# Kernel tuning notes

Measured on AMD Instinct MI355X. Metric: run time of the kernel, lower is better.

Reference implementation:

```python
import jax, jax.numpy as jnp
import numpy as np

N_NODES = 50000
N_EDGES = 800000
D_IN = 128
D_HID = 200
D_OUT = 64
EPS = 0.0  # initial_eps, train_eps=False


def setup_inputs() -> dict:
    key = jax.random.key(0)
    ks = jax.random.split(key, 8)
    x = jax.random.normal(ks[0], (N_NODES, D_IN), dtype=jnp.float32)
    edge_row = jax.random.randint(ks[1], (N_EDGES,), 0, N_NODES)
    edge_col = jax.random.randint(ks[2], (N_EDGES,), 0, N_NODES)
    edge_val = jax.random.uniform(ks[3], (N_EDGES,), dtype=jnp.float32)
    W1 = jax.random.normal(ks[4], (D_IN, D_HID), dtype=jnp.float32) * 0.05
    b1 = jnp.zeros((D_HID,), dtype=jnp.float32)
    W2 = jax.random.normal(ks[5], (D_HID, D_OUT), dtype=jnp.float32) * 0.05
    b2 = jnp.zeros((D_OUT,), dtype=jnp.float32)
    return {"x": x, "edge_row": edge_row, "edge_col": edge_col,
            "edge_val": edge_val, "W1": W1, "b1": b1, "W2": W2, "b2": b2}


def reference(x, edge_row, edge_col, edge_val, W1, b1, W2, b2):
    # SpMM: agg[i] = sum_e val[e] * x[col[e]] for edges with row[e] == i
    msgs = edge_val[:, None] * x[edge_col]            # [E, D_IN] gather
    agg = jax.ops.segment_sum(msgs, edge_row, num_segments=N_NODES)  # [N, D_IN]
    # (1 + eps) * x + A @ x, then 2-layer MLP (Linear -> ReLU -> Linear)
    h = (1.0 + EPS) * x + agg
    h = jax.nn.relu(h @ W1 + b1)                      # [N, D_HID]
    out = h @ W2 + b2                                 # [N, D_OUT]
    return out
```

## Files before the change

kernel.cpp:

```cpp
#include <hip/hip_runtime.h>

#define NN 50000
#define NE 800000
#define DIN 128
#define DH 200
#define DHP 256
#define DO 64
#define RPB 32
#define NBUCK 1564
#define CAP 1024
#define EPB 4096
#define NBLK_E ((NE + EPB - 1) / EPB)
#define CVT_B 3125
#define PACK_B 24

typedef float f32x4 __attribute__((ext_vector_type(4)));
typedef short bf16x8 __attribute__((ext_vector_type(8)));
typedef short s16x4 __attribute__((ext_vector_type(4)));
typedef unsigned int uint;

__device__ __forceinline__ unsigned short f2bf(float f) {
  unsigned int b = __float_as_uint(f);
  b = (b + 0x7FFFu + ((b >> 16) & 1u)) >> 16;
  return (unsigned short)b;
}
__device__ __forceinline__ float bf2f(unsigned short u) {
  return __uint_as_float((unsigned int)u << 16);
}

__global__ __launch_bounds__(256) void k_prep(const float* __restrict__ x,
                                              uint* __restrict__ xb,
                                              const int* __restrict__ row,
                                              int* __restrict__ hist,
                                              const float* __restrict__ W1,
                                              const float* __restrict__ W2,
                                              unsigned short* __restrict__ B1p,
                                              unsigned short* __restrict__ B2p) {
  __shared__ int lh[NBUCK];
  const int bid = blockIdx.x;
  const int tid = threadIdx.x;
  if (bid < CVT_B) {
    int i = bid * 256 + tid;
    f32x4 a = *reinterpret_cast<const f32x4*>(x + (size_t)i * 8);
    f32x4 b = *reinterpret_cast<const f32x4*>(x + (size_t)i * 8 + 4);
    uint4 o;
    o.x = (uint)f2bf(a[0]) | ((uint)f2bf(a[1]) << 16);
    o.y = (uint)f2bf(a[2]) | ((uint)f2bf(a[3]) << 16);
    o.z = (uint)f2bf(b[0]) | ((uint)f2bf(b[1]) << 16);
    o.w = (uint)f2bf(b[2]) | ((uint)f2bf(b[3]) << 16);
    *reinterpret_cast<uint4*>(xb + (size_t)i * 4) = o;
  } else if (bid < CVT_B + NBLK_E) {
    const int hb = bid - CVT_B;
    const int e0 = hb * EPB;
    for (int j = tid; j < NBUCK; j += 256) lh[j] = 0;
    __syncthreads();
#pragma unroll
    for (int p = 0; p < EPB / 256; ++p) {
      int e = e0 + p * 256 + tid;
      if (e < NE) atomicAdd(&lh[row[e] / RPB], 1);
    }
    __syncthreads();
    int* hrow = hist + (size_t)hb * NBUCK;
    for (int j = tid; j < NBUCK; j += 256) hrow[j] = lh[j];
  } else {
    int gidx = (bid - CVT_B - NBLK_E) * 256 + tid;
    if (gidx < 4096) {
      int idx = gidx;
      int lane = idx & 63;
      int s = (idx >> 6) & 3;
      int t = idx >> 8;
      int n = t * 16 + (lane & 15);
      unsigned short v[8];
#pragma unroll
      for (int j = 0; j < 8; ++j) {
        int k = s * 32 + (j & 3) + ((lane >> 4) << 2) + ((j >> 2) << 4);
        float f = (n < DH) ? W1[(size_t)k * DH + n] : 0.f;
        v[j] = f2bf(f);
      }
      *reinterpret_cast<uint4*>(B1p + (size_t)idx * 8) =
          *reinterpret_cast<const uint4*>(v);
    } else {
      int idx = gidx - 4096;
      int lane = idx & 63;
      int s = (idx >> 6) & 7;
      int t = idx >> 9;
      int n = t * 16 + (lane & 15);
      unsigned short v[8];
#pragma unroll
      for (int j = 0; j < 8; ++j) {
        int k = s * 32 + (j & 3) + ((lane >> 4) << 2) + ((j >> 2) << 4);
        float f = (k < DH) ? W2[(size_t)k * DO + n] : 0.f;
        v[j] = f2bf(f);
      }
      *reinterpret_cast<uint4*>(B2p + (size_t)idx * 8) =
          *reinterpret_cast<const uint4*>(v);
    }
  }
}

__global__ __launch_bounds__(256) void k_scanB(int* __restrict__ hist,
                                               int* __restrict__ cnt) {
  __shared__ int ws[4];
  const int k = blockIdx.x;
  const int tid = threadIdx.x;
  int v = (tid < NBLK_E) ? hist[(size_t)tid * NBUCK + k] : 0;
  int lane = tid & 63, wid = tid >> 6;
  int incl = v;
#pragma unroll
  for (int d = 1; d < 64; d <<= 1) {
    int t = __shfl_up(incl, d, 64);
    if (lane >= d) incl += t;
  }
  if (lane == 63) ws[wid] = incl;
  __syncthreads();
  if (tid == 0) {
    int s = 0;
#pragma unroll
    for (int q = 0; q < 4; ++q) { int xx = ws[q]; ws[q] = s; s += xx; }
  }
  __syncthreads();
  int excl = ws[wid] + incl - v;
  if (tid < NBLK_E) hist[(size_t)tid * NBUCK + k] = excl;
  if (tid == 255) cnt[k] = excl;
}

__global__ __launch_bounds__(256) void k_scatC(const int* __restrict__ row,
                                               const int* __restrict__ col,
                                               const float* __restrict__ val,
                                               const int* __restrict__ hist,
                                               uint2* __restrict__ ep) {
  __shared__ int lh[NBUCK];
  __shared__ int lbase[NBUCK];
  const int tid = threadIdx.x;
  const int e0 = blockIdx.x * EPB;
  const int* hrow = hist + (size_t)blockIdx.x * NBUCK;
  for (int j = tid; j < NBUCK; j += 256) { lh[j] = 0; lbase[j] = hrow[j]; }
  __syncthreads();
#pragma unroll
  for (int p = 0; p < EPB / 256; ++p) {
    int e = e0 + p * 256 + tid;
    if (e < NE) {
      int r = row[e];
      int k = r / RPB;
      int rank = atomicAdd(&lh[k], 1);
      int pos = lbase[k] + rank;
      if (pos < CAP)
        ep[(size_t)k * CAP + pos] =
            make_uint2((uint)col[e] | ((uint)(r & (RPB - 1)) << 16),
                       __float_as_uint(val[e]));
    }
  }
}

__global__ __launch_bounds__(256, 8) void k_spmm_mlp(const uint* __restrict__ xbu,
                                                     const uint2* __restrict__ ep,
                                                     const int* __restrict__ cnt,
                                                     const unsigned short* __restrict__ B1p,
                                                     const float* __restrict__ b1,
                                                     const unsigned short* __restrict__ B2p,
                                                     const float* __restrict__ b2,
                                                     float* __restrict__ out) {
  __shared__ uint2 buf2[2112];
  __shared__ int deg[RPB], rbase[RPB], rpos[RPB];
  uint2* se = buf2;
  unsigned short* hb = (unsigned short*)(buf2 + CAP);
  unsigned short* hs = (unsigned short*)buf2;
  const int tid = threadIdx.x;
  const int bucket = blockIdx.x;
  const int r0 = bucket * RPB;
  const int w = tid >> 6, lane = tid & 63;
  const int g = lane >> 4, r16 = lane & 15;
  const int half = lane >> 5, l32 = lane & 31;

  if (tid < RPB) deg[tid] = 0;
  __syncthreads();

  int n = cnt[bucket];
  if (n > CAP) n = CAP;
  const uint2* eb = ep + (size_t)bucket * CAP;

  uint2 rec[4];
  int lr[4];
#pragma unroll
  for (int q = 0; q < 4; ++q) {
    int j = q * 256 + tid;
    rec[q] = (j < n) ? eb[j] : make_uint2(0u, 0u);
    lr[q] = (rec[q].x >> 16) & (RPB - 1);
  }
#pragma unroll
  for (int q = 0; q < 4; ++q)
    if (q * 256 + tid < n) atomicAdd(&deg[lr[q]], 1);
  __syncthreads();

  if (tid < RPB) {
    int v = deg[tid];
    int incl = v;
#pragma unroll
    for (int d = 1; d < RPB; d <<= 1) {
      int t = __shfl_up(incl, d, 64);
      if (tid >= d) incl += t;
    }
    rbase[tid] = incl - v;
    rpos[tid] = incl - v;
  }
  __syncthreads();

#pragma unroll
  for (int q = 0; q < 4; ++q)
    if (q * 256 + tid < n) {
      int p = atomicAdd(&rpos[lr[q]], 1);
      se[p] = make_uint2(rec[q].x & 0xFFFFu, rec[q].y);
    }
  __syncthreads();

  const uint2* xb2 = reinterpret_cast<const uint2*>(xbu);
  for (int rr = w; rr < RPB; rr += 4) {
    int gr = r0 + rr;
    if (gr >= NN) {
      if (half == 0)
        *reinterpret_cast<uint2*>(&hb[rr * 136 + 4 * l32]) = make_uint2(0u, 0u);
      continue;
    }
    int s = rbase[rr];
    int en = s + deg[rr];
    float a0 = 0.f, a1 = 0.f, a2 = 0.f, a3 = 0.f;
    int j = s + half;
    for (; j + 6 < en; j += 8) {
      uint2 e0 = se[j], e1 = se[j + 2], e2 = se[j + 4], e3 = se[j + 6];
      uint2 q0 = xb2[(size_t)e0.x * 32 + l32];
      uint2 q1 = xb2[(size_t)e1.x * 32 + l32];
      uint2 q2 = xb2[(size_t)e2.x * 32 + l32];
      uint2 q3 = xb2[(size_t)e3.x * 32 + l32];
      float v0 = __uint_as_float(e0.y), v1 = __uint_as_float(e1.y);
      float v2 = __uint_as_float(e2.y), v3 = __uint_as_float(e3.y);
      a0 += v0 * bf2f((unsigned short)q0.x) + v1 * bf2f((unsigned short)q1.x) +
            v2 * bf2f((unsigned short)q2.x) + v3 * bf2f((unsigned short)q3.x);
      a1 += v0 * bf2f((unsigned short)(q0.x >> 16)) + v1 * bf2f((unsigned short)(q1.x >> 16)) +
            v2 * bf2f((unsigned short)(q2.x >> 16)) + v3 * bf2f((unsigned short)(q3.x >> 16));
      a2 += v0 * bf2f((unsigned short)q0.y) + v1 * bf2f((unsigned short)q1.y) +
            v2 * bf2f((unsigned short)q2.y) + v3 * bf2f((unsigned short)q3.y);
      a3 += v0 * bf2f((unsigned short)(q0.y >> 16)) + v1 * bf2f((unsigned short)(q1.y >> 16)) +
            v2 * bf2f((unsigned short)(q2.y >> 16)) + v3 * bf2f((unsigned short)(q3.y >> 16));
    }
    for (; j < en; j += 2) {
      uint2 e0 = se[j];
      uint2 q0 = xb2[(size_t)e0.x * 32 + l32];
      float v0 = __uint_as_float(e0.y);
      a0 += v0 * bf2f((unsigned short)q0.x);
      a1 += v0 * bf2f((unsigned short)(q0.x >> 16));
      a2 += v0 * bf2f((unsigned short)q0.y);
      a3 += v0 * bf2f((unsigned short)(q0.y >> 16));
    }
    a0 += __shfl_xor(a0, 32, 64);
    a1 += __shfl_xor(a1, 32, 64);
    a2 += __shfl_xor(a2, 32, 64);
    a3 += __shfl_xor(a3, 32, 64);
    uint2 xs = xb2[(size_t)gr * 32 + l32];
    a0 += bf2f((unsigned short)xs.x);
    a1 += bf2f((unsigned short)(xs.x >> 16));
    a2 += bf2f((unsigned short)xs.y);
    a3 += bf2f((unsigned short)(xs.y >> 16));
    if (half == 0) {
      uint2 o;
      o.x = (uint)f2bf(a0) | ((uint)f2bf(a1) << 16);
      o.y = (uint)f2bf(a2) | ((uint)f2bf(a3) << 16);
      *reinterpret_cast<uint2*>(&hb[rr * 136 + 4 * l32]) = o;
    }
  }
  __syncthreads();

  f32x4 acc[2][4];
#pragma unroll
  for (int a = 0; a < 2; ++a)
#pragma unroll
    for (int b = 0; b < 4; ++b)
#pragma unroll
      for (int c = 0; c < 4; ++c) acc[a][b][c] = 0.f;

  for (int s = 0; s < 4; ++s) {
    bf16x8 af[2];
#pragma unroll
    for (int mr = 0; mr < 2; ++mr) {
      const unsigned short* p = &hb[(mr * 16 + r16) * 136 + s * 32 + g * 4];
      s16x4 lo4 = *reinterpret_cast<const s16x4*>(p);
      s16x4 hi4 = *reinterpret_cast<const s16x4*>(p + 16);
#pragma unroll
      for (int j = 0; j < 4; ++j) { af[mr][j] = lo4[j]; af[mr][4 + j] = hi4[j]; }
    }
#pragma unroll
    for (int nr = 0; nr < 4; ++nr) {
      int t = w * 4 + nr;
      bf16x8 bf = *reinterpret_cast<const bf16x8*>(B1p + (size_t)((t * 4 + s) * 64 + lane) * 8);
      acc[0][nr] = __builtin_amdgcn_mfma_f32_16x16x32_bf16(af[0], bf, acc[0][nr], 0, 0, 0);
      acc[1][nr] = __builtin_amdgcn_mfma_f32_16x16x32_bf16(af[1], bf, acc[1][nr], 0, 0, 0);
    }
  }
  __syncthreads();
#pragma unroll
  for (int mr = 0; mr < 2; ++mr)
#pragma unroll
    for (int nr = 0; nr < 4; ++nr) {
      int nn = w * 64 + nr * 16 + r16;
      float bias = (nn < DH) ? b1[nn] : 0.f;
#pragma unroll
      for (int i = 0; i < 4; ++i) {
        int rl = mr * 16 + g * 4 + i;
        float v = acc[mr][nr][i] + bias;
        v = v > 0.f ? v : 0.f;
        if (nn >= DH) v = 0.f;
        hs[rl * 260 + nn] = f2bf(v);
      }
    }
  __syncthreads();

  f32x4 acc2[2];
#pragma unroll
  for (int b = 0; b < 2; ++b)
#pragma unroll
    for (int c = 0; c < 4; ++c) acc2[b][c] = 0.f;

  for (int s = 0; s < 8; ++s) {
#pragma unroll
    for (int mt = 0; mt < 2; ++mt) {
      const unsigned short* p = &hs[(mt * 16 + r16) * 260 + s * 32 + g * 4];
      s16x4 lo4 = *reinterpret_cast<const s16x4*>(p);
      s16x4 hi4 = *reinterpret_cast<const s16x4*>(p + 16);
      bf16x8 af;
#pragma unroll
      for (int j = 0; j < 4; ++j) { af[j] = lo4[j]; af[4 + j] = hi4[j]; }
      bf16x8 bf = *reinterpret_cast<const bf16x8*>(B2p + (size_t)((w * 8 + s) * 64 + lane) * 8);
      acc2[mt] = __builtin_amdgcn_mfma_f32_16x16x32_bf16(af, bf, acc2[mt], 0, 0, 0);
    }
  }
#pragma unroll
  for (int mt = 0; mt < 2; ++mt) {
    int nn = w * 16 + r16;
    float bias = b2[nn];
#pragma unroll
    for (int i = 0; i < 4; ++i) {
      int grow = r0 + mt * 16 + g * 4 + i;
      if (grow < NN) out[(size_t)grow * DO + nn] = acc2[mt][i] + bias;
    }
  }
}

extern "C" void kernel_launch(void* const* d_in, const int* in_sizes, int n_in,
                              void* d_out, int out_size, void* d_ws, size_t ws_size,
                              hipStream_t stream) {
  const float* x = (const float*)d_in[0];
  const int* erow = (const int*)d_in[1];
  const int* ecol = (const int*)d_in[2];
  const float* eval_ = (const float*)d_in[3];
  const float* W1 = (const float*)d_in[4];
  const float* b1 = (const float*)d_in[5];
  const float* W2 = (const float*)d_in[6];
  const float* b2 = (const float*)d_in[7];
  float* out = (float*)d_out;

  char* ws = (char*)d_ws;
  size_t o = 0;
  uint* xb = (uint*)(ws + o);          o += (size_t)NN * 64 * 4;
  unsigned short* B1p = (unsigned short*)(ws + o); o += 32768 * 2;
  unsigned short* B2p = (unsigned short*)(ws + o); o += 16384 * 2;
  o = (o + 255) & ~(size_t)255;
  int* cnt = (int*)(ws + o);           o += (NBUCK * 4 + 255) & ~(size_t)255;
  int* hist = (int*)(ws + o);          o += (size_t)NBLK_E * NBUCK * 4;
  o = (o + 255) & ~(size_t)255;
  uint2* ep = (uint2*)(ws + o);

  k_prep<<<CVT_B + NBLK_E + PACK_B, 256, 0, stream>>>(x, xb, erow, hist, W1, W2, B1p, B2p);
  k_scanB<<<NBUCK, 256, 0, stream>>>(hist, cnt);
  k_scatC<<<NBLK_E, 256, 0, stream>>>(erow, ecol, eval_, hist, ep);
  k_spmm_mlp<<<NBUCK, 256, 0, stream>>>(xb, ep, cnt, B1p, b1, B2p, b2, out);
}
```

Measured before the change: 78.48 us.

## Halve rows per bucket to 16 for more blocks and smaller LDS

Each bucket now covers 16 rows instead of 32, which doubles the bucket count to 3125 and halves the edge capacity and shared buffer. The fused SpMM+MLP kernel uses one 16-row MFMA tile per wave instead of two and drops the out-of-range row guards, since 50000 divides evenly by 16. Per-row edge end is taken from the next row's base offset instead of the degree array. This is meant to raise block count and occupancy and cut LDS per block, at the cost of loading the B1/B2 weight fragments twice as often per row and a higher risk that a bucket overflows the 512-edge cap.

```diff
diff --git a/kernel.cpp b/kernel.cpp
--- a/kernel.cpp
+++ b/kernel.cpp
@@ -6,9 +6,9 @@
 #define DH 200
 #define DHP 256
 #define DO 64
-#define RPB 32
-#define NBUCK 1564
-#define CAP 1024
+#define RPB 16
+#define NBUCK 3125
+#define CAP 512
 #define EPB 4096
 #define NBLK_E ((NE + EPB - 1) / EPB)
 #define CVT_B 3125
@@ -57,7 +57,7 @@
 #pragma unroll
     for (int p = 0; p < EPB / 256; ++p) {
       int e = e0 + p * 256 + tid;
-      if (e < NE) atomicAdd(&lh[row[e] / RPB], 1);
+      if (e < NE) atomicAdd(&lh[row[e] >> 4], 1);
     }
     __syncthreads();
     int* hrow = hist + (size_t)hb * NBUCK;
@@ -141,7 +141,7 @@
     int e = e0 + p * 256 + tid;
     if (e < NE) {
       int r = row[e];
-      int k = r / RPB;
+      int k = r >> 4;
       int rank = atomicAdd(&lh[k], 1);
       int pos = lbase[k] + rank;
       if (pos < CAP)
@@ -160,7 +160,7 @@
                                                      const unsigned short* __restrict__ B2p,
                                                      const float* __restrict__ b2,
                                                      float* __restrict__ out) {
-  __shared__ uint2 buf2[2112];
+  __shared__ uint2 buf2[1056];
   __shared__ int deg[RPB], rbase[RPB], rpos[RPB];
   uint2* se = buf2;
   unsigned short* hb = (unsigned short*)(buf2 + CAP);
@@ -179,16 +179,16 @@
   if (n > CAP) n = CAP;
   const uint2* eb = ep + (size_t)bucket * CAP;
 
-  uint2 rec[4];
-  int lr[4];
-#pragma unroll
-  for (int q = 0; q < 4; ++q) {
+  uint2 rec[2];
+  int lr[2];
+#pragma unroll
+  for (int q = 0; q < 2; ++q) {
     int j = q * 256 + tid;
     rec[q] = (j < n) ? eb[j] : make_uint2(0u, 0u);
     lr[q] = (rec[q].x >> 16) & (RPB - 1);
   }
 #pragma unroll
-  for (int q = 0; q < 4; ++q)
+  for (int q = 0; q < 2; ++q)
     if (q * 256 + tid < n) atomicAdd(&deg[lr[q]], 1);
   __syncthreads();
 
@@ -206,7 +206,7 @@
   __syncthreads();
 
 #pragma unroll
-  for (int q = 0; q < 4; ++q)
+  for (int q = 0; q < 2; ++q)
     if (q * 256 + tid < n) {
       int p = atomicAdd(&rpos[lr[q]], 1);
       se[p] = make_uint2(rec[q].x & 0xFFFFu, rec[q].y);
@@ -216,13 +216,8 @@
   const uint2* xb2 = reinterpret_cast<const uint2*>(xbu);
   for (int rr = w; rr < RPB; rr += 4) {
     int gr = r0 + rr;
-    if (gr >= NN) {
-      if (half == 0)
-        *reinterpret_cast<uint2*>(&hb[rr * 136 + 4 * l32]) = make_uint2(0u, 0u);
-      continue;
-    }
     int s = rbase[rr];
-    int en = s + deg[rr];
+    int en = (rr < RPB - 1) ? rbase[rr + 1] : n;
     float a0 = 0.f, a1 = 0.f, a2 = 0.f, a3 = 0.f;
     int j = s + half;
     for (; j + 6 < en; j += 8) {
@@ -269,77 +264,63 @@
   }
   __syncthreads();
 
-  f32x4 acc[2][4];
-#pragma unroll
-  for (int a = 0; a < 2; ++a)
-#pragma unroll
-    for (int b = 0; b < 4; ++b)
-#pragma unroll
-      for (int c = 0; c < 4; ++c) acc[a][b][c] = 0.f;
+  f32x4 acc[4];
+#pragma unroll
+  for (int b = 0; b < 4; ++b)
+#pragma unroll
+    for (int c = 0; c < 4; ++c) acc[b][c] = 0.f;
 
   for (int s = 0; s < 4; ++s) {
-    bf16x8 af[2];
-#pragma unroll
-    for (int mr = 0; mr < 2; ++mr) {
-      const unsigned short* p = &hb[(mr * 16 + r16) * 136 + s * 32 + g * 4];
-      s16x4 lo4 = *reinterpret_cast<const s16x4*>(p);
-      s16x4 hi4 = *reinterpret_cast<const s16x4*>(p + 16);
-#pragma unroll
-      for (int j = 0; j < 4; ++j) { af[mr][j] = lo4[j]; af[mr][4 + j] = hi4[j]; }
-    }
+    const unsigned short* p = &hb[r16 * 136 + s * 32 + g * 4];
+    s16x4 lo4 = *reinterpret_cast<const s16x4*>(p);
+    s16x4 hi4 = *reinterpret_cast<const s16x4*>(p + 16);
+    bf16x8 af;
+#pragma unroll
+    for (int j = 0; j < 4; ++j) { af[j] = lo4[j]; af[4 + j] = hi4[j]; }
 #pragma unroll
     for (int nr = 0; nr < 4; ++nr) {
       int t = w * 4 + nr;
       bf16x8 bf = *reinterpret_cast<const bf16x8*>(B1p + (size_t)((t * 4 + s) * 64 + lane) * 8);
-      acc[0][nr] = __builtin_amdgcn_mfma_f32_16x16x32_bf16(af[0], bf, acc[0][nr], 0, 0, 0);
-      acc[1][nr] = __builtin_amdgcn_mfma_f32_16x16x32_bf16(af[1], bf, acc[1][nr], 0, 0, 0);
-    }
-  }
-  __syncthreads();
-#pragma unroll
-  for (int mr = 0; mr < 2; ++mr)
-#pragma unroll
-    for (int nr = 0; nr < 4; ++nr) {
-      int nn = w * 64 + nr * 16 + r16;
-      float bias = (nn < DH) ? b1[nn] : 0.f;
-#pragma unroll
-      for (int i = 0; i < 4; ++i) {
-        int rl = mr * 16 + g * 4 + i;
-        float v = acc[mr][nr][i] + bias;
-        v = v > 0.f ? v : 0.f;
-        if (nn >= DH) v = 0.f;
-        hs[rl * 260 + nn] = f2bf(v);
-      }
-    }
-  __syncthreads();
-
-  f32x4 acc2[2];
-#pragma unroll
-  for (int b = 0; b < 2; ++b)
-#pragma unroll
-    for (int c = 0; c < 4; ++c) acc2[b][c] = 0.f;
+      acc[nr] = __builtin_amdgcn_mfma_f32_16x16x32_bf16(af, bf, acc[nr], 0, 0, 0);
+    }
+  }
+  __syncthreads();
+#pragma unroll
+  for (int nr = 0; nr < 4; ++nr) {
+    int nn = w * 64 + nr * 16 + r16;
+    float bias = (nn < DH) ? b1[nn] : 0.f;
+#pragma unroll
+    for (int i = 0; i < 4; ++i) {
+      int rl = g * 4 + i;
+      float v = acc[nr][i] + bias;
+      v = v > 0.f ? v : 0.f;
+      if (nn >= DH) v = 0.f;
+      hs[rl * 260 + nn] = f2bf(v);
+    }
+  }
+  __syncthreads();
+
+  f32x4 acc2;
+#pragma unroll
+  for (int c = 0; c < 4; ++c) acc2[c] = 0.f;
 
   for (int s = 0; s < 8; ++s) {
-#pragma unroll
-    for (int mt = 0; mt < 2; ++mt) {
-      const unsigned short* p = &hs[(mt * 16 + r16) * 260 + s * 32 + g * 4];
-      s16x4 lo4 = *reinterpret_cast<const s16x4*>(p);
-      s16x4 hi4 = *reinterpret_cast<const s16x4*>(p + 16);
-      bf16x8 af;
-#pragma unroll
-      for (int j = 0; j < 4; ++j) { af[j] = lo4[j]; af[4 + j] = hi4[j]; }
-      bf16x8 bf = *reinterpret_cast<const bf16x8*>(B2p + (size_t)((w * 8 + s) * 64 + lane) * 8);
-      acc2[mt] = __builtin_amdgcn_mfma_f32_16x16x32_bf16(af, bf, acc2[mt], 0, 0, 0);
-    }
-  }
-#pragma unroll
-  for (int mt = 0; mt < 2; ++mt) {
+    const unsigned short* p = &hs[r16 * 260 + s * 32 + g * 4];
+    s16x4 lo4 = *reinterpret_cast<const s16x4*>(p);
+    s16x4 hi4 = *reinterpret_cast<const s16x4*>(p + 16);
+    bf16x8 af;
+#pragma unroll
+    for (int j = 0; j < 4; ++j) { af[j] = lo4[j]; af[4 + j] = hi4[j]; }
+    bf16x8 bf = *reinterpret_cast<const bf16x8*>(B2p + (size_t)((w * 8 + s) * 64 + lane) * 8);
+    acc2 = __builtin_amdgcn_mfma_f32_16x16x32_bf16(af, bf, acc2, 0, 0, 0);
+  }
+  {
     int nn = w * 16 + r16;
     float bias = b2[nn];
 #pragma unroll
     for (int i = 0; i < 4; ++i) {
-      int grow = r0 + mt * 16 + g * 4 + i;
-      if (grow < NN) out[(size_t)grow * DO + nn] = acc2[mt][i] + bias;
+      int grow = r0 + g * 4 + i;
+      out[(size_t)grow * DO + nn] = acc2[i] + bias;
     }
   }
 }
```

Result: slower. 86.64 us (+10.4%).
